# Performance work log

Hardware: AMD Instinct MI355X
Metric: run time of the kernel (lower is better)

Reference implementation:

```python
import jax, jax.numpy as jnp
import numpy as np

B, C, H, W = 8, 256, 128, 128
KC, VC, HEADS = 256, 256, 8


def setup_inputs() -> dict:
    key = jax.random.key(0)
    ks = jax.random.split(key, 10)
    s = 0.05
    return {
        "x": jax.random.normal(ks[0], (B, C, H, W), jnp.float32),
        "Wk": jax.random.normal(ks[1], (KC, C), jnp.float32) * s,
        "bk": jax.random.normal(ks[2], (KC,), jnp.float32) * s,
        "Wq": jax.random.normal(ks[3], (KC, C), jnp.float32) * s,
        "bq": jax.random.normal(ks[4], (KC,), jnp.float32) * s,
        "Wv": jax.random.normal(ks[5], (VC, C), jnp.float32) * s,
        "bv": jax.random.normal(ks[6], (VC,), jnp.float32) * s,
        "Wr": jax.random.normal(ks[7], (C, VC), jnp.float32) * s,
        "br": jax.random.normal(ks[8], (C,), jnp.float32) * s,
        "head_count": HEADS,
    }


def reference(x, Wk, bk, Wq, bq, Wv, bv, Wr, br, head_count):
    n, c, h, w = x.shape
    hw = h * w
    xf = x.reshape(n, c, hw)  # [n, C, S]
    # 1x1 convs == per-pixel linear projections
    keys = jnp.einsum('kc,ncs->nks', Wk, xf) + bk[None, :, None]
    queries = jnp.einsum('kc,ncs->nks', Wq, xf) + bq[None, :, None]
    values = jnp.einsum('vc,ncs->nvs', Wv, xf) + bv[None, :, None]

    dk = Wk.shape[0] // head_count
    dv = Wv.shape[0] // head_count
    # split heads along channel dim (matches torch channel slicing)
    K = jax.nn.softmax(keys.reshape(n, head_count, dk, hw), axis=-1)   # softmax over spatial
    Q = jax.nn.softmax(queries.reshape(n, head_count, dk, hw), axis=2) # softmax over key dim
    V = values.reshape(n, head_count, dv, hw)

    # context = K @ V^T : [n, h, dk, dv]
    ctx = jnp.einsum('nhks,nhvs->nhkv', K, V)
    # attended = ctx^T @ Q : [n, h, dv, S]
    att = jnp.einsum('nhkv,nhks->nhvs', ctx, Q).reshape(n, head_count * dv, h, w)

    attention = jnp.einsum('ov,nvhw->nohw', Wr, att) + br[None, :, None, None]
    # attention map: per-head mean over key dim, then mean over heads
    attention_map = K.mean(axis=2).mean(axis=1).reshape(n, h, w)
    # torch returns the LAST head's context (loop variable after the loop)
    context_last = ctx[:, -1]
    return attention, context_last, attention_map
```

## Files before the change

kernel.cpp:

```cpp
#include <hip/hip_runtime.h>
#include <hip/hip_bf16.h>

typedef float f32x4 __attribute__((ext_vector_type(4)));
typedef short s16x8 __attribute__((ext_vector_type(8)));
typedef short s16x4 __attribute__((ext_vector_type(4)));
typedef __bf16 bf16x8 __attribute__((ext_vector_type(8)));
typedef unsigned short u16;

#define DEVI __device__ __forceinline__

static constexpr int    HW      = 16384;
static constexpr size_t BSTRIDE = (size_t)256 * HW;

static constexpr size_t oXBT   = 0;
static constexpr size_t oEK    = oXBT  + (size_t)8 * HW * 256 * 2;
static constexpr size_t oQT    = oEK   + (size_t)8 * 256 * HW * 2;
static constexpr size_t oVB    = oQT   + (size_t)8 * HW * 256 * 2;
static constexpr size_t oWK    = oVB   + (size_t)8 * 256 * HW * 2;
static constexpr size_t oBIAS  = oWK   + (size_t)768 * 256 * 2;
static constexpr size_t oISE   = oBIAS + 4096;
static constexpr size_t oPS    = oISE  + 8192;
static constexpr size_t oCTX   = oPS   + (size_t)256 * 2048 * 4;
static constexpr size_t oMB    = oCTX  + (size_t)64 * 1024 * 4;
static constexpr size_t oCPART = oMB   + (size_t)8 * 256 * 256 * 2;
static constexpr size_t oMPART = oCPART + (size_t)4096 * 1024 * 4;

DEVI float bf2f(short x) {
  unsigned u = ((unsigned)(unsigned short)x) << 16;
  return __builtin_bit_cast(float, u);
}
DEVI u16 f2bf(float x) { return __builtin_bit_cast(u16, (__bf16)x); }

DEVI void gld16(const void* g, void* l) {
  __builtin_amdgcn_global_load_lds(
      (__attribute__((address_space(1))) void*)(g),
      (__attribute__((address_space(3))) void*)(l), 16, 0, 0);
}

__global__ __launch_bounds__(256) void k_prep(
    const float* __restrict__ Wk, const float* __restrict__ Wq, const float* __restrict__ Wv,
    const float* __restrict__ bk, const float* __restrict__ bq, const float* __restrict__ bv,
    u16* __restrict__ Wkqv, float* __restrict__ bias)
{
  int i = blockIdx.x * 256 + threadIdx.x;
  for (int p = i; p < 768 * 256; p += 64 * 256) {
    float v = (p < 65536) ? Wk[p] : (p < 131072 ? Wq[p - 65536] : Wv[p - 131072]);
    Wkqv[p] = f2bf(v);
  }
  if (i < 768) bias[i] = (i < 256) ? bk[i] : (i < 512 ? bq[i - 256] : bv[i - 512]);
}

__global__ __launch_bounds__(256) void k_transpose(const float* __restrict__ in_, u16* __restrict__ out)
{
  __shared__ u16 lds[64 * 256];
  const int t = threadIdx.x;
  const int n = blockIdx.y;
  const int s0 = blockIdx.x * 64;
  const float* src = in_ + ((size_t)n * 256 + t) * HW + s0;
  #pragma unroll
  for (int i = 0; i < 16; ++i) {
    f32x4 v = *(const f32x4*)(src + i * 4);
    #pragma unroll
    for (int j = 0; j < 4; ++j) lds[(i * 4 + j) * 256 + t] = f2bf(v[j]);
  }
  __syncthreads();
  s16x8* gp = (s16x8*)(out + (size_t)n * BSTRIDE + (size_t)s0 * 256);
  const s16x8* lp = (const s16x8*)lds;
  #pragma unroll
  for (int i = 0; i < 8; ++i) gp[t + i * 256] = lp[t + i * 256];
}


__global__ __launch_bounds__(256, 2) void k_projKV(
    const u16* __restrict__ W, const u16* __restrict__ xbT, const float* __restrict__ bias,
    u16* __restrict__ ek, u16* __restrict__ vb, float* __restrict__ ps)
{
  __shared__ u16 smem[32768];
  const int t = threadIdx.x;
  const int L = blockIdx.x;
  const int n = L & 7;
  const int idx = L >> 3;
  const int mbi = idx & 3;
  const int sq  = idx >> 2;
  const bool isK = (mbi < 2);
  const int m0 = (mbi & 1) * 128;
  const int aBase = (isK ? 0 : 512) + m0;
  const int lane = t & 63;
  const int l15 = lane & 15, l4 = (lane >> 4) & 3;
  const int wv = t >> 6;
  const int wm = (wv & 1) * 64, wn = (wv >> 1) * 64;
  const u16* Ab = W + (size_t)aBase * 256;
  const u16* Bb = xbT + (size_t)n * BSTRIDE;
  u16* Al = smem;
  u16* Bl = smem + 16384;

  float biasv[4];
  #pragma unroll
  for (int mf = 0; mf < 4; ++mf) biasv[mf] = bias[aBase + wm + mf * 16 + l15];

  const int rr = t >> 3;
  const int csh = t & 7;
  auto STAGE = [&](int buf, int it) {
    const int k0 = (it & 3) * 64;
    const size_t s_t0 = (size_t)((sq * 4 + (it >> 2)) * 128);
    #pragma unroll
    for (int i = 0; i < 4; ++i) {
      const int row = i * 32 + rr;
      const int cs = (csh ^ (row & 7)) * 8;
      gld16(Ab + (size_t)row * 256 + k0 + cs,          Al + buf * 8192 + i * 2048 + t * 8);
      gld16(Bb + (s_t0 + row) * 256 + k0 + cs,         Bl + buf * 8192 + i * 2048 + t * 8);
    }
  };

  f32x4 acc[4][4] = {};
  STAGE(0, 0); STAGE(1, 1);

  u16* outb = (isK ? ek : vb) + (size_t)n * BSTRIDE;

  #pragma unroll
  for (int it = 0; it < 16; ++it) {
    if (it == 15)                          asm volatile("s_waitcnt vmcnt(0)" ::: "memory");
    else if ((it & 3) <= 1 && it >= 4) {
      if (isK) asm volatile("s_waitcnt vmcnt(28)" ::: "memory");
      else     asm volatile("s_waitcnt vmcnt(24)" ::: "memory");
    } else                                 asm volatile("s_waitcnt vmcnt(8)" ::: "memory");
    __builtin_amdgcn_s_barrier();

    const int buf = it & 1;
    #pragma unroll
    for (int ks = 0; ks < 2; ++ks) {
      bf16x8 af[4], bff[4];
      #pragma unroll
      for (int g = 0; g < 4; ++g) {
        const int mrow = wm + g * 16 + l15;
        const int srow = wn + g * 16 + l15;
        af[g]  = *(const bf16x8*)&Al[buf * 8192 + mrow * 64 + (((ks * 4 + l4) ^ (mrow & 7)) * 8)];
        bff[g] = *(const bf16x8*)&Bl[buf * 8192 + srow * 64 + (((ks * 4 + l4) ^ (srow & 7)) * 8)];
      }
      __builtin_amdgcn_s_setprio(1);
      #pragma unroll
      for (int sf = 0; sf < 4; ++sf)
        #pragma unroll
        for (int mf = 0; mf < 4; ++mf)
          acc[sf][mf] = __builtin_amdgcn_mfma_f32_16x16x32_bf16(bff[sf], af[mf], acc[sf][mf], 0, 0, 0);
      __builtin_amdgcn_s_setprio(0);
    }
    asm volatile("s_waitcnt lgkmcnt(0)" ::: "memory");
    __builtin_amdgcn_s_barrier();
    if (it < 14) STAGE(buf, it + 2);

    if ((it & 3) == 3) {
      const int tile = it >> 2;
      const int s0t = (sq * 4 + tile) * 128;
      const int stile = sq * 4 + tile;
      if (isK) {
        float rs[4] = {0.f, 0.f, 0.f, 0.f};
        #pragma unroll
        for (int sf = 0; sf < 4; ++sf)
          #pragma unroll
          for (int mf = 0; mf < 4; ++mf) {
            s16x4 pk;
            #pragma unroll
            for (int r = 0; r < 4; ++r) {
              const float e = __expf(acc[sf][mf][r] + biasv[mf]);
              rs[mf] += e;
              pk[r] = (short)f2bf(e);
            }
            *(s16x4*)(outb + (size_t)(m0 + wm + mf * 16 + l15) * HW + s0t + wn + sf * 16 + l4 * 4) = pk;
          }
        #pragma unroll
        for (int mf = 0; mf < 4; ++mf) {
          float v = rs[mf];
          v += __shfl_xor(v, 16); v += __shfl_xor(v, 32);
          if (l4 == 0)
            ps[((size_t)(stile * 2 + (wn >> 6))) * 2048 + n * 256 + m0 + wm + mf * 16 + l15] = v;
        }
      } else {
        #pragma unroll
        for (int sf = 0; sf < 4; ++sf)
          #pragma unroll
          for (int mf = 0; mf < 4; ++mf) {
            s16x4 pk;
            #pragma unroll
            for (int r = 0; r < 4; ++r) pk[r] = (short)f2bf(acc[sf][mf][r] + biasv[mf]);
            *(s16x4*)(outb + (size_t)(m0 + wm + mf * 16 + l15) * HW + s0t + wn + sf * 16 + l4 * 4) = pk;
          }
      }
      #pragma unroll
      for (int sf = 0; sf < 4; ++sf)
        #pragma unroll
        for (int mf = 0; mf < 4; ++mf) acc[sf][mf] = f32x4{0.f, 0.f, 0.f, 0.f};
    }
  }
}

__global__ __launch_bounds__(256, 2) void k_attn2(
    const u16* __restrict__ Mb, const u16* __restrict__ qT, const float* __restrict__ br,
    float* __restrict__ Out)
{
  __shared__ u16 smem[32768];
  const int t = threadIdx.x;
  const int L = blockIdx.x;
  const int n = L & 7;
  const int idx = L >> 3;
  const int mb = idx & 1;
  const int sq = idx >> 1;
  const int m0 = mb * 128;
  const int lane = t & 63;
  const int l15 = lane & 15, l4 = (lane >> 4) & 3;
  const int wv = t >> 6;
  const int wm = (wv & 1) * 64, wn = (wv >> 1) * 64;
  const u16* Ab = Mb + (size_t)n * 65536 + (size_t)m0 * 256;
  const u16* Bb = qT + (size_t)n * BSTRIDE;
  u16* Al = smem;
  u16* Bl = smem + 16384;

  float biasv[4];
  #pragma unroll
  for (int mf = 0; mf < 4; ++mf) biasv[mf] = br[m0 + wm + mf * 16 + l15];

  const int rr = t >> 3;
  const int csh = t & 7;
  auto STAGE = [&](int buf, int it) {
    const int k0 = (it & 3) * 64;
    const size_t s_t0 = (size_t)((sq * 4 + (it >> 2)) * 128);
    #pragma unroll
    for (int i = 0; i < 4; ++i) {
      const int row = i * 32 + rr;
      const int cs = (csh ^ (row & 7)) * 8;
      gld16(Ab + (size_t)row * 256 + k0 + cs,  Al + buf * 8192 + i * 2048 + t * 8);
      gld16(Bb + (s_t0 + row) * 256 + k0 + cs, Bl + buf * 8192 + i * 2048 + t * 8);
    }
  };

  f32x4 acc[4][4] = {};
  STAGE(0, 0); STAGE(1, 1);

  float* ob = Out + (size_t)n * BSTRIDE;

  #pragma unroll
  for (int it = 0; it < 16; ++it) {
    if (it == 15)                          asm volatile("s_waitcnt vmcnt(0)" ::: "memory");
    else if ((it & 3) <= 1 && it >= 4)     asm volatile("s_waitcnt vmcnt(24)" ::: "memory");
    else                                   asm volatile("s_waitcnt vmcnt(8)" ::: "memory");
    __builtin_amdgcn_s_barrier();

    const int buf = it & 1;
    #pragma unroll
    for (int ks = 0; ks < 2; ++ks) {
      bf16x8 af[4], bff[4];
      #pragma unroll
      for (int g = 0; g < 4; ++g) {
        const int mrow = wm + g * 16 + l15;
        const int srow = wn + g * 16 + l15;
        af[g]  = *(const bf16x8*)&Al[buf * 8192 + mrow * 64 + (((ks * 4 + l4) ^ (mrow & 7)) * 8)];
        bff[g] = *(const bf16x8*)&Bl[buf * 8192 + srow * 64 + (((ks * 4 + l4) ^ (srow & 7)) * 8)];
      }
      __builtin_amdgcn_s_setprio(1);
      #pragma unroll
      for (int sf = 0; sf < 4; ++sf)
        #pragma unroll
        for (int mf = 0; mf < 4; ++mf)
          acc[sf][mf] = __builtin_amdgcn_mfma_f32_16x16x32_bf16(bff[sf], af[mf], acc[sf][mf], 0, 0, 0);
      __builtin_amdgcn_s_setprio(0);
    }
    asm volatile("s_waitcnt lgkmcnt(0)" ::: "memory");
    __builtin_amdgcn_s_barrier();
    if (it < 14) STAGE(buf, it + 2);

    if ((it & 3) == 3) {
      const int s0t = (sq * 4 + (it >> 2)) * 128;
      #pragma unroll
      for (int sf = 0; sf < 4; ++sf)
        #pragma unroll
        for (int mf = 0; mf < 4; ++mf) {
          f32x4 o = acc[sf][mf] + biasv[mf];
          *(f32x4*)(ob + (size_t)(m0 + wm + mf * 16 + l15) * HW + s0t + wn + sf * 16 + l4 * 4) = o;
          acc[sf][mf] = f32x4{0.f, 0.f, 0.f, 0.f};
        }
    }
  }
}

#define GEMM_CORE(Ab, Bb)                                                                   \
  u16* Al = smem;                                                                           \
  u16* Bl = smem + 16384;                                                                   \
  auto STAGE = [&](int buf, int kt) {                                                       \
    const int k0 = kt * 64;                                                                 \
    _Pragma("unroll")                                                                       \
    for (int i = 0; i < 4; ++i) {                                                           \
      const int r_ = i * 32 + (t >> 3);                                                     \
      const int cs = (((t & 7) ^ (r_ & 7)) * 8);                                            \
      gld16((Ab) + (size_t)r_ * 256 + k0 + cs, Al + buf * 8192 + i * 2048 + t * 8);         \
      gld16((Bb) + (size_t)r_ * 256 + k0 + cs, Bl + buf * 8192 + i * 2048 + t * 8);         \
    }                                                                                       \
  };                                                                                        \
  f32x4 acc[4][4] = {};                                                                     \
  STAGE(0, 0); STAGE(1, 1);                                                                 \
  _Pragma("unroll")                                                                         \
  for (int kt = 0; kt < 4; ++kt) {                                                          \
    if (kt < 3) asm volatile("s_waitcnt vmcnt(8)" ::: "memory");                            \
    else        asm volatile("s_waitcnt vmcnt(0)" ::: "memory");                            \
    __builtin_amdgcn_s_barrier();                                                           \
    const int buf = kt & 1;                                                                 \
    _Pragma("unroll")                                                                       \
    for (int ks = 0; ks < 2; ++ks) {                                                        \
      bf16x8 af[4], bff[4];                                                                 \
      _Pragma("unroll")                                                                     \
      for (int g = 0; g < 4; ++g) {                                                         \
        const int mrow = wm + g * 16 + l15;                                                 \
        const int srow = wn + g * 16 + l15;                                                 \
        af[g]  = *(const bf16x8*)&Al[buf * 8192 + mrow * 64 + (((ks * 4 + l4) ^ (mrow & 7)) * 8)]; \
        bff[g] = *(const bf16x8*)&Bl[buf * 8192 + srow * 64 + (((ks * 4 + l4) ^ (srow & 7)) * 8)]; \
      }                                                                                     \
      __builtin_amdgcn_s_setprio(1);                                                        \
      _Pragma("unroll")                                                                     \
      for (int mg = 0; mg < 4; ++mg)                                                        \
        _Pragma("unroll")                                                                   \
        for (int ng = 0; ng < 4; ++ng)                                                      \
          acc[mg][ng] = __builtin_amdgcn_mfma_f32_16x16x32_bf16(af[mg], bff[ng], acc[mg][ng], 0, 0, 0); \
      __builtin_amdgcn_s_setprio(0);                                                        \
    }                                                                                       \
    asm volatile("s_waitcnt lgkmcnt(0)" ::: "memory");                                      \
    __builtin_amdgcn_s_barrier();                                                           \
    if (kt < 2) STAGE(buf, kt + 2);                                                         \
  }

__global__ __launch_bounds__(256, 2) void k_projQ(
    const u16* __restrict__ W, const u16* __restrict__ xbT, const float* __restrict__ bias,
    u16* __restrict__ qT)
{
  __shared__ u16 smem[32768];
  const int t = threadIdx.x;
  const int L = blockIdx.x;
  const int n  = L & 7;
  const int idx = L >> 3;
  const int mbq = idx & 1;
  const int sb  = idx >> 1;
  const int m0 = 256 + mbq * 128, s0 = sb * 128;
  const int lane = t & 63;
  const int l15 = lane & 15, l4 = (lane >> 4) & 3;
  const int wv = t >> 6;
  const int wm = (wv & 1) * 64, wn = (wv >> 1) * 64;
  const u16* Ab = W + (size_t)m0 * 256;
  const u16* Bb = xbT + (size_t)n * BSTRIDE + (size_t)s0 * 256;

  GEMM_CORE(Ab, Bb)

  #pragma unroll
  for (int mg = 0; mg < 4; ++mg)
    #pragma unroll
    for (int r = 0; r < 4; ++r) {
      const float bb = bias[m0 + wm + mg * 16 + l4 * 4 + r];
      #pragma unroll
      for (int ng = 0; ng < 4; ++ng) acc[mg][ng][r] += bb;
    }

  #pragma unroll
  for (int hh = 0; hh < 2; ++hh)
    #pragma unroll
    for (int ng = 0; ng < 4; ++ng) {
      float s = 0.f;
      #pragma unroll
      for (int mg = hh * 2; mg < hh * 2 + 2; ++mg)
        #pragma unroll
        for (int r = 0; r < 4; ++r) { const float e = __expf(acc[mg][ng][r]); acc[mg][ng][r] = e; s += e; }
      s += __shfl_xor(s, 16);
      s += __shfl_xor(s, 32);
      const float inv = 1.f / s;
      #pragma unroll
      for (int mg = hh * 2; mg < hh * 2 + 2; ++mg)
        #pragma unroll
        for (int r = 0; r < 4; ++r) acc[mg][ng][r] *= inv;
    }
  __syncthreads();
  #pragma unroll
  for (int mg = 0; mg < 4; ++mg)
    #pragma unroll
    for (int ng = 0; ng < 4; ++ng)
      #pragma unroll
      for (int r = 0; r < 4; ++r) {
        const int srow = wn + ng * 16 + l15;
        const int mcol = wm + mg * 16 + l4 * 4 + r;
        smem[srow * 136 + mcol] = f2bf(acc[mg][ng][r]);
      }
  __syncthreads();
  u16* O = qT + (size_t)n * BSTRIDE + (size_t)s0 * 256 + mbq * 128;
  #pragma unroll
  for (int it = 0; it < 8; ++it) {
    const int row = it * 16 + (t >> 4);
    *(s16x8*)(O + (size_t)row * 256 + (t & 15) * 8) = *(const s16x8*)&smem[row * 136 + (t & 15) * 8];
  }
}

__global__ __launch_bounds__(256) void k_inv(const float* __restrict__ ps, float* __restrict__ ise)
{
  const int i = blockIdx.x * 256 + threadIdx.x;
  float s = 0.f;
  for (int b = 0; b < 256; ++b) s += ps[(size_t)b * 2048 + i];
  ise[i] = 1.f / s;
}

__global__ __launch_bounds__(64) void k_ctx_part(
    const u16* __restrict__ ek, const u16* __restrict__ vb, const float* __restrict__ ise,
    float* __restrict__ cpart, float* __restrict__ mpart)
{
  const int blk = blockIdx.x;
  const int chunk = blk & 63, nh = blk >> 6;
  const int h = nh & 7, n = nh >> 3;
  const int lane = threadIdx.x;
  const int l15 = lane & 15, l4 = lane >> 4;
  const u16* kb = ek + ((size_t)n * 256 + h * 32) * HW;
  const u16* vv = vb + ((size_t)n * 256 + h * 32) * HW;
  const float iv0 = ise[n * 256 + h * 32 + l15];
  const float iv1 = ise[n * 256 + h * 32 + 16 + l15];
  f32x4 acc[2][2] = {};
  float macc[8][8] = {};
  const int sbase = chunk * 256 + l4 * 8;
  #pragma unroll
  for (int ks = 0; ks < 8; ++ks) {
    const int sb = sbase + ks * 32;
    bf16x8 ef[2], vf[2];
    #pragma unroll
    for (int g = 0; g < 2; ++g) {
      ef[g] = *(const bf16x8*)(kb + (size_t)(g * 16 + l15) * HW + sb);
      vf[g] = *(const bf16x8*)(vv + (size_t)(g * 16 + l15) * HW + sb);
    }
    #pragma unroll
    for (int j = 0; j < 8; ++j)
      macc[ks][j] = fmaf(iv0, (float)ef[0][j], fmaf(iv1, (float)ef[1][j], macc[ks][j]));
    #pragma unroll
    for (int a = 0; a < 2; ++a)
      #pragma unroll
      for (int b = 0; b < 2; ++b)
        acc[a][b] = __builtin_amdgcn_mfma_f32_16x16x32_bf16(ef[a], vf[b], acc[a][b], 0, 0, 0);
  }
  float* op = cpart + (size_t)blk * 1024;
  #pragma unroll
  for (int a = 0; a < 2; ++a)
    #pragma unroll
    for (int b = 0; b < 2; ++b)
      #pragma unroll
      for (int r = 0; r < 4; ++r)
        op[(a * 16 + l4 * 4 + r) * 32 + b * 16 + l15] = acc[a][b][r];
  #pragma unroll
  for (int ks = 0; ks < 8; ++ks)
    #pragma unroll
    for (int j = 0; j < 8; ++j) {
      float v = macc[ks][j];
      v += __shfl_xor(v, 1); v += __shfl_xor(v, 2);
      v += __shfl_xor(v, 4); v += __shfl_xor(v, 8);
      macc[ks][j] = v;
    }
  if (l15 == 0) {
    float* mp = mpart + ((size_t)h * 8 + n) * HW + sbase;
    #pragma unroll
    for (int ks = 0; ks < 8; ++ks) {
      f32x4 a = {macc[ks][0], macc[ks][1], macc[ks][2], macc[ks][3]};
      f32x4 b = {macc[ks][4], macc[ks][5], macc[ks][6], macc[ks][7]};
      *(f32x4*)(mp + ks * 32)     = a;
      *(f32x4*)(mp + ks * 32 + 4) = b;
    }
  }
}

__global__ __launch_bounds__(256) void k_ctx_reduce(
    const float* __restrict__ cpart, const float* __restrict__ ise,
    float* __restrict__ ctx, float* __restrict__ dctx)
{
  const int nh = blockIdx.x, n = nh >> 3, h = nh & 7, t = threadIdx.x;
  f32x4 a = {};
  for (int c = 0; c < 64; ++c) a += *(const f32x4*)(cpart + ((size_t)nh * 64 + c) * 1024 + t * 4);
  const float inv = ise[n * 256 + h * 32 + (t >> 3)];
  a *= inv;
  *(f32x4*)(ctx + (size_t)nh * 1024 + t * 4) = a;
  if (h == 7) *(f32x4*)(dctx + (size_t)n * 1024 + t * 4) = a;
}

__global__ __launch_bounds__(256) void k_mmat(
    const float* __restrict__ ctx, const float* __restrict__ Wr, u16* __restrict__ Mb)
{
  const int nh = blockIdx.x, n = nh >> 3, h = nh & 7, o = threadIdx.x;
  __shared__ float cl[1024];
  #pragma unroll
  for (int i = 0; i < 4; ++i) cl[o + i * 256] = ctx[(size_t)nh * 1024 + o + i * 256];
  __syncthreads();
  float wr[32];
  const float* wp = Wr + (size_t)o * 256 + h * 32;
  #pragma unroll
  for (int v = 0; v < 32; ++v) wr[v] = wp[v];
  u16* mp = Mb + ((size_t)n * 256 + o) * 256 + h * 32;
  #pragma unroll 4
  for (int k = 0; k < 32; ++k) {
    float s = 0.f;
    #pragma unroll
    for (int v = 0; v < 32; ++v) s += wr[v] * cl[k * 32 + v];
    mp[k] = f2bf(s);
  }
}

__global__ __launch_bounds__(256) void k_map_reduce(const float* __restrict__ mpart, float* __restrict__ dmap)
{
  const int i = blockIdx.x * 256 + threadIdx.x;
  f32x4 a = {};
  #pragma unroll
  for (int h = 0; h < 8; ++h) a += *(const f32x4*)(mpart + (size_t)h * 131072 + (size_t)i * 4);
  a *= (1.0f / 256.0f);
  *(f32x4*)(dmap + (size_t)i * 4) = a;
}

extern "C" void kernel_launch(void* const* d_in, const int* in_sizes, int n_in,
                              void* d_out, int out_size, void* d_ws, size_t ws_size,
                              hipStream_t stream)
{
  (void)in_sizes; (void)n_in; (void)out_size; (void)ws_size;
  const float* x  = (const float*)d_in[0];
  const float* Wk = (const float*)d_in[1];
  const float* bk = (const float*)d_in[2];
  const float* Wq = (const float*)d_in[3];
  const float* bq = (const float*)d_in[4];
  const float* Wv = (const float*)d_in[5];
  const float* bv = (const float*)d_in[6];
  const float* Wr = (const float*)d_in[7];
  const float* br = (const float*)d_in[8];

  char* ws = (char*)d_ws;
  u16*   xbT  = (u16*)(ws + oXBT);
  u16*   ek   = (u16*)(ws + oEK);
  u16*   qT   = (u16*)(ws + oQT);
  u16*   vb   = (u16*)(ws + oVB);
  u16*   Wkqv = (u16*)(ws + oWK);
  float* bias = (float*)(ws + oBIAS);
  float* ise  = (float*)(ws + oISE);
  float* ps   = (float*)(ws + oPS);
  float* ctx  = (float*)(ws + oCTX);
  u16*   Mb   = (u16*)(ws + oMB);
  float* cpart= (float*)(ws + oCPART);
  float* mpart= (float*)(ws + oMPART);

  float* attn = (float*)d_out;
  float* dctx = (float*)d_out + 33554432;
  float* dmap = (float*)d_out + 33562624;

  k_prep<<<64, 256, 0, stream>>>(Wk, Wq, Wv, bk, bq, bv, Wkqv, bias);
  k_transpose<<<dim3(256, 8), 256, 0, stream>>>(x, xbT);
  k_projKV<<<1024, 256, 0, stream>>>(Wkqv, xbT, bias, ek, vb, ps);
  k_inv<<<8, 256, 0, stream>>>(ps, ise);
  k_projQ<<<2048, 256, 0, stream>>>(Wkqv, xbT, bias, qT);
  k_ctx_part<<<4096, 64, 0, stream>>>(ek, vb, ise, cpart, mpart);
  k_ctx_reduce<<<64, 256, 0, stream>>>(cpart, ise, ctx, dctx);
  k_mmat<<<64, 256, 0, stream>>>(ctx, Wr, Mb);
  k_map_reduce<<<128, 256, 0, stream>>>(mpart, dmap);
  k_attn2<<<512, 256, 0, stream>>>(Mb, qT, br, attn);
}
```

Before: 289.7 us.

## Merge small launches into combined prep, projection and post-processing kernels

Folds weight conversion into the transpose kernel and merges the K/V and Q projection GEMMs into a single launch, with the block index choosing the branch. It also combines the context reduction, the Wr mixing matrix and the attention-map reduction into one post kernel, so the intermediate ctx buffer goes away. The launch count drops from ten to six, cutting per-launch overhead and tail idle time between kernels. The risk is that the merged projection kernel's register use and occupancy are set by the heavier branch, and the k_inv launch still sits between the projection and k_ctx_part.

```diff
diff --git a/kernel.cpp b/kernel.cpp
--- a/kernel.cpp
+++ b/kernel.cpp
@@ -37,248 +37,37 @@
       (__attribute__((address_space(3))) void*)(l), 16, 0, 0);
 }
 
-__global__ __launch_bounds__(256) void k_prep(
+__global__ __launch_bounds__(256) void k_pt(
+    const float* __restrict__ x,
     const float* __restrict__ Wk, const float* __restrict__ Wq, const float* __restrict__ Wv,
     const float* __restrict__ bk, const float* __restrict__ bq, const float* __restrict__ bv,
-    u16* __restrict__ Wkqv, float* __restrict__ bias)
-{
-  int i = blockIdx.x * 256 + threadIdx.x;
-  for (int p = i; p < 768 * 256; p += 64 * 256) {
-    float v = (p < 65536) ? Wk[p] : (p < 131072 ? Wq[p - 65536] : Wv[p - 131072]);
-    Wkqv[p] = f2bf(v);
-  }
-  if (i < 768) bias[i] = (i < 256) ? bk[i] : (i < 512 ? bq[i - 256] : bv[i - 512]);
-}
-
-__global__ __launch_bounds__(256) void k_transpose(const float* __restrict__ in_, u16* __restrict__ out)
+    u16* __restrict__ xbT, u16* __restrict__ Wkqv, float* __restrict__ bias)
 {
   __shared__ u16 lds[64 * 256];
   const int t = threadIdx.x;
-  const int n = blockIdx.y;
-  const int s0 = blockIdx.x * 64;
-  const float* src = in_ + ((size_t)n * 256 + t) * HW + s0;
-  #pragma unroll
-  for (int i = 0; i < 16; ++i) {
-    f32x4 v = *(const f32x4*)(src + i * 4);
-    #pragma unroll
-    for (int j = 0; j < 4; ++j) lds[(i * 4 + j) * 256 + t] = f2bf(v[j]);
-  }
-  __syncthreads();
-  s16x8* gp = (s16x8*)(out + (size_t)n * BSTRIDE + (size_t)s0 * 256);
-  const s16x8* lp = (const s16x8*)lds;
-  #pragma unroll
-  for (int i = 0; i < 8; ++i) gp[t + i * 256] = lp[t + i * 256];
-}
-
-
-__global__ __launch_bounds__(256, 2) void k_projKV(
-    const u16* __restrict__ W, const u16* __restrict__ xbT, const float* __restrict__ bias,
-    u16* __restrict__ ek, u16* __restrict__ vb, float* __restrict__ ps)
-{
-  __shared__ u16 smem[32768];
-  const int t = threadIdx.x;
-  const int L = blockIdx.x;
-  const int n = L & 7;
-  const int idx = L >> 3;
-  const int mbi = idx & 3;
-  const int sq  = idx >> 2;
-  const bool isK = (mbi < 2);
-  const int m0 = (mbi & 1) * 128;
-  const int aBase = (isK ? 0 : 512) + m0;
-  const int lane = t & 63;
-  const int l15 = lane & 15, l4 = (lane >> 4) & 3;
-  const int wv = t >> 6;
-  const int wm = (wv & 1) * 64, wn = (wv >> 1) * 64;
-  const u16* Ab = W + (size_t)aBase * 256;
-  const u16* Bb = xbT + (size_t)n * BSTRIDE;
-  u16* Al = smem;
-  u16* Bl = smem + 16384;
-
-  float biasv[4];
-  #pragma unroll
-  for (int mf = 0; mf < 4; ++mf) biasv[mf] = bias[aBase + wm + mf * 16 + l15];
-
-  const int rr = t >> 3;
-  const int csh = t & 7;
-  auto STAGE = [&](int buf, int it) {
-    const int k0 = (it & 3) * 64;
-    const size_t s_t0 = (size_t)((sq * 4 + (it >> 2)) * 128);
-    #pragma unroll
-    for (int i = 0; i < 4; ++i) {
-      const int row = i * 32 + rr;
-      const int cs = (csh ^ (row & 7)) * 8;
-      gld16(Ab + (size_t)row * 256 + k0 + cs,          Al + buf * 8192 + i * 2048 + t * 8);
-      gld16(Bb + (s_t0 + row) * 256 + k0 + cs,         Bl + buf * 8192 + i * 2048 + t * 8);
-    }
-  };
-
-  f32x4 acc[4][4] = {};
-  STAGE(0, 0); STAGE(1, 1);
-
-  u16* outb = (isK ? ek : vb) + (size_t)n * BSTRIDE;
-
-  #pragma unroll
-  for (int it = 0; it < 16; ++it) {
-    if (it == 15)                          asm volatile("s_waitcnt vmcnt(0)" ::: "memory");
-    else if ((it & 3) <= 1 && it >= 4) {
-      if (isK) asm volatile("s_waitcnt vmcnt(28)" ::: "memory");
-      else     asm volatile("s_waitcnt vmcnt(24)" ::: "memory");
-    } else                                 asm volatile("s_waitcnt vmcnt(8)" ::: "memory");
-    __builtin_amdgcn_s_barrier();
-
-    const int buf = it & 1;
-    #pragma unroll
-    for (int ks = 0; ks < 2; ++ks) {
-      bf16x8 af[4], bff[4];
-      #pragma unroll
-      for (int g = 0; g < 4; ++g) {
-        const int mrow = wm + g * 16 + l15;
-        const int srow = wn + g * 16 + l15;
-        af[g]  = *(const bf16x8*)&Al[buf * 8192 + mrow * 64 + (((ks * 4 + l4) ^ (mrow & 7)) * 8)];
-        bff[g] = *(const bf16x8*)&Bl[buf * 8192 + srow * 64 + (((ks * 4 + l4) ^ (srow & 7)) * 8)];
-      }
-      __builtin_amdgcn_s_setprio(1);
-      #pragma unroll
-      for (int sf = 0; sf < 4; ++sf)
-        #pragma unroll
-        for (int mf = 0; mf < 4; ++mf)
-          acc[sf][mf] = __builtin_amdgcn_mfma_f32_16x16x32_bf16(bff[sf], af[mf], acc[sf][mf], 0, 0, 0);
-      __builtin_amdgcn_s_setprio(0);
-    }
-    asm volatile("s_waitcnt lgkmcnt(0)" ::: "memory");
-    __builtin_amdgcn_s_barrier();
-    if (it < 14) STAGE(buf, it + 2);
-
-    if ((it & 3) == 3) {
-      const int tile = it >> 2;
-      const int s0t = (sq * 4 + tile) * 128;
-      const int stile = sq * 4 + tile;
-      if (isK) {
-        float rs[4] = {0.f, 0.f, 0.f, 0.f};
-        #pragma unroll
-        for (int sf = 0; sf < 4; ++sf)
-          #pragma unroll
-          for (int mf = 0; mf < 4; ++mf) {
-            s16x4 pk;
-            #pragma unroll
-            for (int r = 0; r < 4; ++r) {
-              const float e = __expf(acc[sf][mf][r] + biasv[mf]);
-              rs[mf] += e;
-              pk[r] = (short)f2bf(e);
-            }
-            *(s16x4*)(outb + (size_t)(m0 + wm + mf * 16 + l15) * HW + s0t + wn + sf * 16 + l4 * 4) = pk;
-          }
-        #pragma unroll
-        for (int mf = 0; mf < 4; ++mf) {
-          float v = rs[mf];
-          v += __shfl_xor(v, 16); v += __shfl_xor(v, 32);
-          if (l4 == 0)
-            ps[((size_t)(stile * 2 + (wn >> 6))) * 2048 + n * 256 + m0 + wm + mf * 16 + l15] = v;
-        }
-      } else {
-        #pragma unroll
-        for (int sf = 0; sf < 4; ++sf)
-          #pragma unroll
-          for (int mf = 0; mf < 4; ++mf) {
-            s16x4 pk;
-            #pragma unroll
-            for (int r = 0; r < 4; ++r) pk[r] = (short)f2bf(acc[sf][mf][r] + biasv[mf]);
-            *(s16x4*)(outb + (size_t)(m0 + wm + mf * 16 + l15) * HW + s0t + wn + sf * 16 + l4 * 4) = pk;
-          }
-      }
-      #pragma unroll
-      for (int sf = 0; sf < 4; ++sf)
-        #pragma unroll
-        for (int mf = 0; mf < 4; ++mf) acc[sf][mf] = f32x4{0.f, 0.f, 0.f, 0.f};
-    }
-  }
-}
-
-__global__ __launch_bounds__(256, 2) void k_attn2(
-    const u16* __restrict__ Mb, const u16* __restrict__ qT, const float* __restrict__ br,
-    float* __restrict__ Out)
-{
-  __shared__ u16 smem[32768];
-  const int t = threadIdx.x;
-  const int L = blockIdx.x;
-  const int n = L & 7;
-  const int idx = L >> 3;
-  const int mb = idx & 1;
-  const int sq = idx >> 1;
-  const int m0 = mb * 128;
-  const int lane = t & 63;
-  const int l15 = lane & 15, l4 = (lane >> 4) & 3;
-  const int wv = t >> 6;
-  const int wm = (wv & 1) * 64, wn = (wv >> 1) * 64;
-  const u16* Ab = Mb + (size_t)n * 65536 + (size_t)m0 * 256;
-  const u16* Bb = qT + (size_t)n * BSTRIDE;
-  u16* Al = smem;
-  u16* Bl = smem + 16384;
-
-  float biasv[4];
-  #pragma unroll
-  for (int mf = 0; mf < 4; ++mf) biasv[mf] = br[m0 + wm + mf * 16 + l15];
-
-  const int rr = t >> 3;
-  const int csh = t & 7;
-  auto STAGE = [&](int buf, int it) {
-    const int k0 = (it & 3) * 64;
-    const size_t s_t0 = (size_t)((sq * 4 + (it >> 2)) * 128);
-    #pragma unroll
-    for (int i = 0; i < 4; ++i) {
-      const int row = i * 32 + rr;
-      const int cs = (csh ^ (row & 7)) * 8;
-      gld16(Ab + (size_t)row * 256 + k0 + cs,  Al + buf * 8192 + i * 2048 + t * 8);
-      gld16(Bb + (s_t0 + row) * 256 + k0 + cs, Bl + buf * 8192 + i * 2048 + t * 8);
-    }
-  };
-
-  f32x4 acc[4][4] = {};
-  STAGE(0, 0); STAGE(1, 1);
-
-  float* ob = Out + (size_t)n * BSTRIDE;
-
-  #pragma unroll
-  for (int it = 0; it < 16; ++it) {
-    if (it == 15)                          asm volatile("s_waitcnt vmcnt(0)" ::: "memory");
-    else if ((it & 3) <= 1 && it >= 4)     asm volatile("s_waitcnt vmcnt(24)" ::: "memory");
-    else                                   asm volatile("s_waitcnt vmcnt(8)" ::: "memory");
-    __builtin_amdgcn_s_barrier();
-
-    const int buf = it & 1;
-    #pragma unroll
-    for (int ks = 0; ks < 2; ++ks) {
-      bf16x8 af[4], bff[4];
-      #pragma unroll
-      for (int g = 0; g < 4; ++g) {
-        const int mrow = wm + g * 16 + l15;
-        const int srow = wn + g * 16 + l15;
-        af[g]  = *(const bf16x8*)&Al[buf * 8192 + mrow * 64 + (((ks * 4 + l4) ^ (mrow & 7)) * 8)];
-        bff[g] = *(const bf16x8*)&Bl[buf * 8192 + srow * 64 + (((ks * 4 + l4) ^ (srow & 7)) * 8)];
-      }
-      __builtin_amdgcn_s_setprio(1);
-      #pragma unroll
-      for (int sf = 0; sf < 4; ++sf)
-        #pragma unroll
-        for (int mf = 0; mf < 4; ++mf)
-          acc[sf][mf] = __builtin_amdgcn_mfma_f32_16x16x32_bf16(bff[sf], af[mf], acc[sf][mf], 0, 0, 0);
-      __builtin_amdgcn_s_setprio(0);
-    }
-    asm volatile("s_waitcnt lgkmcnt(0)" ::: "memory");
-    __builtin_amdgcn_s_barrier();
-    if (it < 14) STAGE(buf, it + 2);
-
-    if ((it & 3) == 3) {
-      const int s0t = (sq * 4 + (it >> 2)) * 128;
-      #pragma unroll
-      for (int sf = 0; sf < 4; ++sf)
-        #pragma unroll
-        for (int mf = 0; mf < 4; ++mf) {
-          f32x4 o = acc[sf][mf] + biasv[mf];
-          *(f32x4*)(ob + (size_t)(m0 + wm + mf * 16 + l15) * HW + s0t + wn + sf * 16 + l4 * 4) = o;
-          acc[sf][mf] = f32x4{0.f, 0.f, 0.f, 0.f};
-        }
-    }
+  const int tb = blockIdx.x;
+  if (tb < 2048) {
+    const int n = tb >> 8;
+    const int s0 = (tb & 255) * 64;
+    const float* src = x + ((size_t)n * 256 + t) * HW + s0;
+    #pragma unroll
+    for (int i = 0; i < 16; ++i) {
+      f32x4 v = *(const f32x4*)(src + i * 4);
+      #pragma unroll
+      for (int j = 0; j < 4; ++j) lds[(i * 4 + j) * 256 + t] = f2bf(v[j]);
+    }
+    __syncthreads();
+    s16x8* gp = (s16x8*)(xbT + (size_t)n * BSTRIDE + (size_t)s0 * 256);
+    const s16x8* lp = (const s16x8*)lds;
+    #pragma unroll
+    for (int i = 0; i < 8; ++i) gp[t + i * 256] = lp[t + i * 256];
+  } else {
+    const int i = (tb - 2048) * 256 + t;
+    for (int p = i; p < 768 * 256; p += 64 * 256) {
+      float v = (p < 65536) ? Wk[p] : (p < 131072 ? Wq[p - 65536] : Wv[p - 131072]);
+      Wkqv[p] = f2bf(v);
+    }
+    if (i < 768) bias[i] = (i < 256) ? bk[i] : (i < 512 ? bq[i - 256] : bv[i - 512]);
   }
 }
 
@@ -326,70 +115,182 @@
     if (kt < 2) STAGE(buf, kt + 2);                                                         \
   }
 
-__global__ __launch_bounds__(256, 2) void k_projQ(
+__global__ __launch_bounds__(256, 2) void k_proj(
     const u16* __restrict__ W, const u16* __restrict__ xbT, const float* __restrict__ bias,
-    u16* __restrict__ qT)
+    u16* __restrict__ ek, u16* __restrict__ qT, u16* __restrict__ vb, float* __restrict__ ps)
 {
   __shared__ u16 smem[32768];
   const int t = threadIdx.x;
   const int L = blockIdx.x;
-  const int n  = L & 7;
+  const int n = L & 7;
   const int idx = L >> 3;
-  const int mbq = idx & 1;
-  const int sb  = idx >> 1;
-  const int m0 = 256 + mbq * 128, s0 = sb * 128;
   const int lane = t & 63;
   const int l15 = lane & 15, l4 = (lane >> 4) & 3;
   const int wv = t >> 6;
   const int wm = (wv & 1) * 64, wn = (wv >> 1) * 64;
-  const u16* Ab = W + (size_t)m0 * 256;
-  const u16* Bb = xbT + (size_t)n * BSTRIDE + (size_t)s0 * 256;
-
-  GEMM_CORE(Ab, Bb)
-
-  #pragma unroll
-  for (int mg = 0; mg < 4; ++mg)
-    #pragma unroll
-    for (int r = 0; r < 4; ++r) {
-      const float bb = bias[m0 + wm + mg * 16 + l4 * 4 + r];
-      #pragma unroll
-      for (int ng = 0; ng < 4; ++ng) acc[mg][ng][r] += bb;
-    }
-
-  #pragma unroll
-  for (int hh = 0; hh < 2; ++hh)
-    #pragma unroll
-    for (int ng = 0; ng < 4; ++ng) {
-      float s = 0.f;
-      #pragma unroll
-      for (int mg = hh * 2; mg < hh * 2 + 2; ++mg)
-        #pragma unroll
-        for (int r = 0; r < 4; ++r) { const float e = __expf(acc[mg][ng][r]); acc[mg][ng][r] = e; s += e; }
-      s += __shfl_xor(s, 16);
-      s += __shfl_xor(s, 32);
-      const float inv = 1.f / s;
-      #pragma unroll
-      for (int mg = hh * 2; mg < hh * 2 + 2; ++mg)
-        #pragma unroll
-        for (int r = 0; r < 4; ++r) acc[mg][ng][r] *= inv;
-    }
-  __syncthreads();
-  #pragma unroll
-  for (int mg = 0; mg < 4; ++mg)
-    #pragma unroll
-    for (int ng = 0; ng < 4; ++ng)
+
+  if (idx < 128) {
+    const int mbi = idx & 3;
+    const int sq  = idx >> 2;
+    const bool isK = (mbi < 2);
+    const int m0 = (mbi & 1) * 128;
+    const int aBase = (isK ? 0 : 512) + m0;
+    const u16* Ab = W + (size_t)aBase * 256;
+    const u16* Bb = xbT + (size_t)n * BSTRIDE;
+    u16* Al = smem;
+    u16* Bl = smem + 16384;
+
+    float biasv[4];
+    #pragma unroll
+    for (int mf = 0; mf < 4; ++mf) biasv[mf] = bias[aBase + wm + mf * 16 + l15];
+
+    const int rr = t >> 3;
+    const int csh = t & 7;
+    auto STAGE = [&](int buf, int it) {
+      const int k0 = (it & 3) * 64;
+      const size_t s_t0 = (size_t)((sq * 4 + (it >> 2)) * 128);
+      #pragma unroll
+      for (int i = 0; i < 4; ++i) {
+        const int row = i * 32 + rr;
+        const int cs = (csh ^ (row & 7)) * 8;
+        gld16(Ab + (size_t)row * 256 + k0 + cs,  Al + buf * 8192 + i * 2048 + t * 8);
+        gld16(Bb + (s_t0 + row) * 256 + k0 + cs, Bl + buf * 8192 + i * 2048 + t * 8);
+      }
+    };
+
+    f32x4 acc[4][4] = {};
+    STAGE(0, 0); STAGE(1, 1);
+    u16* outb = (isK ? ek : vb) + (size_t)n * BSTRIDE;
+
+    #pragma unroll
+    for (int it = 0; it < 16; ++it) {
+      if (it == 15)                          asm volatile("s_waitcnt vmcnt(0)" ::: "memory");
+      else if ((it & 3) <= 1 && it >= 4) {
+        if (isK) asm volatile("s_waitcnt vmcnt(28)" ::: "memory");
+        else     asm volatile("s_waitcnt vmcnt(24)" ::: "memory");
+      } else                                 asm volatile("s_waitcnt vmcnt(8)" ::: "memory");
+      __builtin_amdgcn_s_barrier();
+
+      const int buf = it & 1;
+      #pragma unroll
+      for (int ks = 0; ks < 2; ++ks) {
+        bf16x8 af[4], bff[4];
+        #pragma unroll
+        for (int g = 0; g < 4; ++g) {
+          const int mrow = wm + g * 16 + l15;
+          const int srow = wn + g * 16 + l15;
+          af[g]  = *(const bf16x8*)&Al[buf * 8192 + mrow * 64 + (((ks * 4 + l4) ^ (mrow & 7)) * 8)];
+          bff[g] = *(const bf16x8*)&Bl[buf * 8192 + srow * 64 + (((ks * 4 + l4) ^ (srow & 7)) * 8)];
+        }
+        __builtin_amdgcn_s_setprio(1);
+        #pragma unroll
+        for (int sf = 0; sf < 4; ++sf)
+          #pragma unroll
+          for (int mf = 0; mf < 4; ++mf)
+            acc[sf][mf] = __builtin_amdgcn_mfma_f32_16x16x32_bf16(bff[sf], af[mf], acc[sf][mf], 0, 0, 0);
+        __builtin_amdgcn_s_setprio(0);
+      }
+      asm volatile("s_waitcnt lgkmcnt(0)" ::: "memory");
+      __builtin_amdgcn_s_barrier();
+      if (it < 14) STAGE(buf, it + 2);
+
+      if ((it & 3) == 3) {
+        const int tile = it >> 2;
+        const int s0t = (sq * 4 + tile) * 128;
+        const int stile = sq * 4 + tile;
+        if (isK) {
+          float rs[4] = {0.f, 0.f, 0.f, 0.f};
+          #pragma unroll
+          for (int sf = 0; sf < 4; ++sf)
+            #pragma unroll
+            for (int mf = 0; mf < 4; ++mf) {
+              s16x4 pk;
+              #pragma unroll
+              for (int r = 0; r < 4; ++r) {
+                const float e = __expf(acc[sf][mf][r] + biasv[mf]);
+                rs[mf] += e;
+                pk[r] = (short)f2bf(e);
+              }
+              *(s16x4*)(outb + (size_t)(m0 + wm + mf * 16 + l15) * HW + s0t + wn + sf * 16 + l4 * 4) = pk;
+            }
+          #pragma unroll
+          for (int mf = 0; mf < 4; ++mf) {
+            float v = rs[mf];
+            v += __shfl_xor(v, 16); v += __shfl_xor(v, 32);
+            if (l4 == 0)
+              ps[((size_t)(stile * 2 + (wn >> 6))) * 2048 + n * 256 + m0 + wm + mf * 16 + l15] = v;
+          }
+        } else {
+          #pragma unroll
+          for (int sf = 0; sf < 4; ++sf)
+            #pragma unroll
+            for (int mf = 0; mf < 4; ++mf) {
+              s16x4 pk;
+              #pragma unroll
+              for (int r = 0; r < 4; ++r) pk[r] = (short)f2bf(acc[sf][mf][r] + biasv[mf]);
+              *(s16x4*)(outb + (size_t)(m0 + wm + mf * 16 + l15) * HW + s0t + wn + sf * 16 + l4 * 4) = pk;
+            }
+        }
+        #pragma unroll
+        for (int sf = 0; sf < 4; ++sf)
+          #pragma unroll
+          for (int mf = 0; mf < 4; ++mf) acc[sf][mf] = f32x4{0.f, 0.f, 0.f, 0.f};
+      }
+    }
+  } else {
+    const int qidx = idx - 128;
+    const int mbq = qidx & 1;
+    const int sb  = qidx >> 1;
+    const int m0 = 256 + mbq * 128, s0 = sb * 128;
+    const u16* Ab = W + (size_t)m0 * 256;
+    const u16* Bb = xbT + (size_t)n * BSTRIDE + (size_t)s0 * 256;
+
+    GEMM_CORE(Ab, Bb)
+
+    #pragma unroll
+    for (int mg = 0; mg < 4; ++mg)
       #pragma unroll
       for (int r = 0; r < 4; ++r) {
-        const int srow = wn + ng * 16 + l15;
-        const int mcol = wm + mg * 16 + l4 * 4 + r;
-        smem[srow * 136 + mcol] = f2bf(acc[mg][ng][r]);
+        const float bb = bias[m0 + wm + mg * 16 + l4 * 4 + r];
+        #pragma unroll
+        for (int ng = 0; ng < 4; ++ng) acc[mg][ng][r] += bb;
       }
-  __syncthreads();
-  u16* O = qT + (size_t)n * BSTRIDE + (size_t)s0 * 256 + mbq * 128;
-  #pragma unroll
-  for (int it = 0; it < 8; ++it) {
-    const int row = it * 16 + (t >> 4);
-    *(s16x8*)(O + (size_t)row * 256 + (t & 15) * 8) = *(const s16x8*)&smem[row * 136 + (t & 15) * 8];
+
+    #pragma unroll
+    for (int hh = 0; hh < 2; ++hh)
+      #pragma unroll
+      for (int ng = 0; ng < 4; ++ng) {
+        float s = 0.f;
+        #pragma unroll
+        for (int mg = hh * 2; mg < hh * 2 + 2; ++mg)
+          #pragma unroll
+          for (int r = 0; r < 4; ++r) { const float e = __expf(acc[mg][ng][r]); acc[mg][ng][r] = e; s += e; }
+        s += __shfl_xor(s, 16);
+        s += __shfl_xor(s, 32);
+        const float inv = 1.f / s;
+        #pragma unroll
+        for (int mg = hh * 2; mg < hh * 2 + 2; ++mg)
+          #pragma unroll
+          for (int r = 0; r < 4; ++r) acc[mg][ng][r] *= inv;
+      }
+    __syncthreads();
+    #pragma unroll
+    for (int mg = 0; mg < 4; ++mg)
+      #pragma unroll
+      for (int ng = 0; ng < 4; ++ng)
+        #pragma unroll
+        for (int r = 0; r < 4; ++r) {
+          const int srow = wn + ng * 16 + l15;
+          const int mcol = wm + mg * 16 + l4 * 4 + r;
+          smem[srow * 136 + mcol] = f2bf(acc[mg][ng][r]);
+        }
+    __syncthreads();
+    u16* O = qT + (size_t)n * BSTRIDE + (size_t)s0 * 256 + mbq * 128;
+    #pragma unroll
+    for (int it = 0; it < 8; ++it) {
+      const int row = it * 16 + (t >> 4);
+      *(s16x8*)(O + (size_t)row * 256 + (t & 15) * 8) = *(const s16x8*)&smem[row * 136 + (t & 15) * 8];
+    }
   }
 }
 
@@ -464,49 +365,131 @@
   }
 }
 
-__global__ __launch_bounds__(256) void k_ctx_reduce(
+__global__ __launch_bounds__(256) void k_post(
     const float* __restrict__ cpart, const float* __restrict__ ise,
-    float* __restrict__ ctx, float* __restrict__ dctx)
-{
-  const int nh = blockIdx.x, n = nh >> 3, h = nh & 7, t = threadIdx.x;
-  f32x4 a = {};
-  for (int c = 0; c < 64; ++c) a += *(const f32x4*)(cpart + ((size_t)nh * 64 + c) * 1024 + t * 4);
-  const float inv = ise[n * 256 + h * 32 + (t >> 3)];
-  a *= inv;
-  *(f32x4*)(ctx + (size_t)nh * 1024 + t * 4) = a;
-  if (h == 7) *(f32x4*)(dctx + (size_t)n * 1024 + t * 4) = a;
-}
-
-__global__ __launch_bounds__(256) void k_mmat(
-    const float* __restrict__ ctx, const float* __restrict__ Wr, u16* __restrict__ Mb)
-{
-  const int nh = blockIdx.x, n = nh >> 3, h = nh & 7, o = threadIdx.x;
-  __shared__ float cl[1024];
+    const float* __restrict__ Wr, const float* __restrict__ mpart,
+    u16* __restrict__ Mb, float* __restrict__ dctx, float* __restrict__ dmap)
+{
+  const int t = threadIdx.x;
+  if (blockIdx.x < 64) {
+    const int nh = blockIdx.x, n = nh >> 3, h = nh & 7;
+    __shared__ float cl[1024];
+    f32x4 a = {};
+    for (int c = 0; c < 64; ++c) a += *(const f32x4*)(cpart + ((size_t)nh * 64 + c) * 1024 + t * 4);
+    const float inv = ise[n * 256 + h * 32 + (t >> 3)];
+    a *= inv;
+    *(f32x4*)(cl + t * 4) = a;
+    if (h == 7) *(f32x4*)(dctx + (size_t)n * 1024 + t * 4) = a;
+    __syncthreads();
+    const int o = t;
+    float wr[32];
+    const float* wp = Wr + (size_t)o * 256 + h * 32;
+    #pragma unroll
+    for (int v = 0; v < 32; ++v) wr[v] = wp[v];
+    u16* mp = Mb + ((size_t)n * 256 + o) * 256 + h * 32;
+    #pragma unroll 4
+    for (int k = 0; k < 32; ++k) {
+      float s = 0.f;
+      #pragma unroll
+      for (int v = 0; v < 32; ++v) s += wr[v] * cl[k * 32 + v];
+      mp[k] = f2bf(s);
+    }
+  } else {
+    const int i = (blockIdx.x - 64) * 256 + t;
+    f32x4 a = {};
+    #pragma unroll
+    for (int h = 0; h < 8; ++h) a += *(const f32x4*)(mpart + (size_t)h * 131072 + (size_t)i * 4);
+    a *= (1.0f / 256.0f);
+    *(f32x4*)(dmap + (size_t)i * 4) = a;
+  }
+}
+
+__global__ __launch_bounds__(256, 2) void k_attn2(
+    const u16* __restrict__ Mb, const u16* __restrict__ qT, const float* __restrict__ br,
+    float* __restrict__ Out)
+{
+  __shared__ u16 smem[32768];
+  const int t = threadIdx.x;
+  const int L = blockIdx.x;
+  const int n = L & 7;
+  const int idx = L >> 3;
+  const int mb = idx & 1;
+  const int sq = idx >> 1;
+  const int m0 = mb * 128;
+  const int lane = t & 63;
+  const int l15 = lane & 15, l4 = (lane >> 4) & 3;
+  const int wv = t >> 6;
+  const int wm = (wv & 1) * 64, wn = (wv >> 1) * 64;
+  const u16* Ab = Mb + (size_t)n * 65536 + (size_t)m0 * 256;
+  const u16* Bb = qT + (size_t)n * BSTRIDE;
+  u16* Al = smem;
+  u16* Bl = smem + 16384;
+
+  float biasv[4];
   #pragma unroll
-  for (int i = 0; i < 4; ++i) cl[o + i * 256] = ctx[(size_t)nh * 1024 + o + i * 256];
-  __syncthreads();
-  float wr[32];
-  const float* wp = Wr + (size_t)o * 256 + h * 32;
+  for (int mf = 0; mf < 4; ++mf) biasv[mf] = br[m0 + wm + mf * 16 + l15];
+
+  const int rr = t >> 3;
+  const int csh = t & 7;
+  auto STAGE = [&](int buf, int it) {
+    const int k0 = (it & 3) * 64;
+    const size_t s_t0 = (size_t)((sq * 4 + (it >> 2)) * 128);
+    #pragma unroll
+    for (int i = 0; i < 4; ++i) {
+      const int row = i * 32 + rr;
+      const int cs = (csh ^ (row & 7)) * 8;
+      gld16(Ab + (size_t)row * 256 + k0 + cs,  Al + buf * 8192 + i * 2048 + t * 8);
+      gld16(Bb + (s_t0 + row) * 256 + k0 + cs, Bl + buf * 8192 + i * 2048 + t * 8);
+    }
+  };
+
+  f32x4 acc[4][4] = {};
+  STAGE(0, 0); STAGE(1, 1);
+
+  float* ob = Out + (size_t)n * BSTRIDE;
+
   #pragma unroll
-  for (int v = 0; v < 32; ++v) wr[v] = wp[v];
-  u16* mp = Mb + ((size_t)n * 256 + o) * 256 + h * 32;
-  #pragma unroll 4
-  for (int k = 0; k < 32; ++k) {
-    float s = 0.f;
-    #pragma unroll
-    for (int v = 0; v < 32; ++v) s += wr[v] * cl[k * 32 + v];
-    mp[k] = f2bf(s);
-  }
-}
-
-__global__ __launch_bounds__(256) void k_map_reduce(const float* __restrict__ mpart, float* __restrict__ dmap)
-{
-  const int i = blockIdx.x * 256 + threadIdx.x;
-  f32x4 a = {};
-  #pragma unroll
-  for (int h = 0; h < 8; ++h) a += *(const f32x4*)(mpart + (size_t)h * 131072 + (size_t)i * 4);
-  a *= (1.0f / 256.0f);
-  *(f32x4*)(dmap + (size_t)i * 4) = a;
+  for (int it = 0; it < 16; ++it) {
+    if (it == 15)                          asm volatile("s_waitcnt vmcnt(0)" ::: "memory");
+    else if ((it & 3) <= 1 && it >= 4)     asm volatile("s_waitcnt vmcnt(24)" ::: "memory");
+    else                                   asm volatile("s_waitcnt vmcnt(8)" ::: "memory");
+    __builtin_amdgcn_s_barrier();
+
+    const int buf = it & 1;
+    #pragma unroll
+    for (int ks = 0; ks < 2; ++ks) {
+      bf16x8 af[4], bff[4];
+      #pragma unroll
+      for (int g = 0; g < 4; ++g) {
+        const int mrow = wm + g * 16 + l15;
+        const int srow = wn + g * 16 + l15;
+        af[g]  = *(const bf16x8*)&Al[buf * 8192 + mrow * 64 + (((ks * 4 + l4) ^ (mrow & 7)) * 8)];
+        bff[g] = *(const bf16x8*)&Bl[buf * 8192 + srow * 64 + (((ks * 4 + l4) ^ (srow & 7)) * 8)];
+      }
+      __builtin_amdgcn_s_setprio(1);
+      #pragma unroll
+      for (int sf = 0; sf < 4; ++sf)
+        #pragma unroll
+        for (int mf = 0; mf < 4; ++mf)
+          acc[sf][mf] = __builtin_amdgcn_mfma_f32_16x16x32_bf16(bff[sf], af[mf], acc[sf][mf], 0, 0, 0);
+      __builtin_amdgcn_s_setprio(0);
+    }
+    asm volatile("s_waitcnt lgkmcnt(0)" ::: "memory");
+    __builtin_amdgcn_s_barrier();
+    if (it < 14) STAGE(buf, it + 2);
+
+    if ((it & 3) == 3) {
+      const int s0t = (sq * 4 + (it >> 2)) * 128;
+      #pragma unroll
+      for (int sf = 0; sf < 4; ++sf)
+        #pragma unroll
+        for (int mf = 0; mf < 4; ++mf) {
+          f32x4 o = acc[sf][mf] + biasv[mf];
+          *(f32x4*)(ob + (size_t)(m0 + wm + mf * 16 + l15) * HW + s0t + wn + sf * 16 + l4 * 4) = o;
+          acc[sf][mf] = f32x4{0.f, 0.f, 0.f, 0.f};
+        }
+    }
+  }
 }
 
 extern "C" void kernel_launch(void* const* d_in, const int* in_sizes, int n_in,
@@ -533,7 +516,6 @@
   float* bias = (float*)(ws + oBIAS);
   float* ise  = (float*)(ws + oISE);
   float* ps   = (float*)(ws + oPS);
-  float* ctx  = (float*)(ws + oCTX);
   u16*   Mb   = (u16*)(ws + oMB);
   float* cpart= (float*)(ws + oCPART);
   float* mpart= (float*)(ws + oMPART);
@@ -542,14 +524,10 @@
   float* dctx = (float*)d_out + 33554432;
   float* dmap = (float*)d_out + 33562624;
 
-  k_prep<<<64, 256, 0, stream>>>(Wk, Wq, Wv, bk, bq, bv, Wkqv, bias);
-  k_transpose<<<dim3(256, 8), 256, 0, stream>>>(x, xbT);
-  k_projKV<<<1024, 256, 0, stream>>>(Wkqv, xbT, bias, ek, vb, ps);
+  k_pt<<<2112, 256, 0, stream>>>(x, Wk, Wq, Wv, bk, bq, bv, xbT, Wkqv, bias);
+  k_proj<<<3072, 256, 0, stream>>>(Wkqv, xbT, bias, ek, qT, vb, ps);
   k_inv<<<8, 256, 0, stream>>>(ps, ise);
-  k_projQ<<<2048, 256, 0, stream>>>(Wkqv, xbT, bias, qT);
   k_ctx_part<<<4096, 64, 0, stream>>>(ek, vb, ise, cpart, mpart);
-  k_ctx_reduce<<<64, 256, 0, stream>>>(cpart, ise, ctx, dctx);
-  k_mmat<<<64, 256, 0, stream>>>(ctx, Wr, Mb);
-  k_map_reduce<<<128, 256, 0, stream>>>(mpart, dmap);
+  k_post<<<192, 256, 0, stream>>>(cpart, ise, Wr, mpart, Mb, dctx, dmap);
   k_attn2<<<512, 256, 0, stream>>>(Mb, qT, br, attn);
 }
```

Result: faster. 283.8 us (-2.0%).
